# Kernel tuning notes

Hardware: AMD Instinct MI355X
Metric: run time of the kernel (lower is better)

## Reference

```python
import jax, jax.numpy as jnp
import numpy as np

N, E, F_IN, H, O = 50000, 800000, 128, 64, 1


def _gcn_conv(x, row, col, ew, W, b, n_nodes):
    """PyG GCNConv: add self-loops (weight 1), symmetric deg normalization,
    linear transform (no bias inside lin), scatter-add aggregation, then +bias."""
    loop = jnp.arange(n_nodes, dtype=row.dtype)
    r = jnp.concatenate([row, loop])
    c = jnp.concatenate([col, loop])
    w = jnp.concatenate([ew, jnp.ones((n_nodes,), dtype=ew.dtype)])
    deg = jax.ops.segment_sum(w, c, num_segments=n_nodes)            # [N]
    dis = jnp.where(deg > 0, jax.lax.rsqrt(jnp.maximum(deg, 1e-12)), 0.0)
    norm = dis[r] * w * dis[c]                                       # [E+N]
    h = x @ W                                                        # [N, out]
    msg = h[r] * norm[:, None]                                       # gather + scale
    agg = jax.ops.segment_sum(msg, c, num_segments=n_nodes)          # scatter-add
    return agg + b


def setup_inputs() -> dict:
    key = jax.random.key(0)
    ks = jax.random.split(key, 14)
    s = 0.02
    return {
        "x": jax.random.normal(ks[0], (N, F_IN), dtype=jnp.float32),
        "edge_index": jax.random.randint(ks[1], (2, E), 0, N, dtype=jnp.int64),
        "edge_weight": jax.random.uniform(ks[2], (E,), dtype=jnp.float32),
        "W1": jax.random.normal(ks[3], (F_IN, H), dtype=jnp.float32) * s,
        "b1": jnp.zeros((H,), dtype=jnp.float32),
        "W2": jax.random.normal(ks[4], (H, H), dtype=jnp.float32) * s,
        "b2": jnp.zeros((H,), dtype=jnp.float32),
        "W_ih": jax.random.normal(ks[5], (4 * H, H), dtype=jnp.float32) * s,
        "W_hh": jax.random.normal(ks[6], (4 * H, H), dtype=jnp.float32) * s,
        "b_ih": jax.random.normal(ks[7], (4 * H,), dtype=jnp.float32) * s,
        "b_hh": jax.random.normal(ks[8], (4 * H,), dtype=jnp.float32) * s,
        "W_reg": jax.random.normal(ks[9], (H, O), dtype=jnp.float32) * s,
        "b_reg": jnp.zeros((O,), dtype=jnp.float32),
    }


def reference(x, edge_index, edge_weight, W1, b1, W2, b2,
              W_ih, W_hh, b_ih, b_hh, W_reg, b_reg):
    row, col = edge_index[0], edge_index[1]
    n = x.shape[0]
    h = jax.nn.relu(_gcn_conv(x, row, col, edge_weight, W1, b1, n))
    h = jax.nn.relu(_gcn_conv(h, row, col, edge_weight, W2, b2, n))
    # single-step LSTM, zero initial (h0, c0); PyTorch gate order i, f, g, o
    hd = W_ih.shape[1]
    h0 = jnp.zeros((n, hd), dtype=h.dtype)
    gates = h @ W_ih.T + h0 @ W_hh.T + b_ih + b_hh                   # [N, 4H]
    i, f, g, o = jnp.split(gates, 4, axis=-1)
    c = jax.nn.sigmoid(f) * 0.0 + jax.nn.sigmoid(i) * jnp.tanh(g)    # c0 = 0
    hn = jax.nn.sigmoid(o) * jnp.tanh(c)                             # lstm_out[:, -1]
    return hn @ W_reg + b_reg
```

## Files before the change

kernel.cpp:

```cpp
#include <hip/hip_runtime.h>
#include <math.h>


#define QN 6272
#define NOCT 8
#define NPAD (NOCT * QN)
#define NSLICE 128
#define HIST_BLOCKS (NSLICE * NOCT)

__device__ __forceinline__ float sigmoidf_(float x) {
    return 1.0f / (1.0f + expf(-x));
}

__global__ __launch_bounds__(256) void hist_gemm1_k(
        const int* __restrict__ col, unsigned short* __restrict__ part,
        int E, int N,
        const float* __restrict__ x, const float* __restrict__ W1,
        float* __restrict__ C) {
    extern __shared__ char smem[];
    const int t = threadIdx.x;
    if (blockIdx.x < HIST_BLOCKS) {
        int* hc = (int*)smem;
        const int s = blockIdx.x >> 3;
        const int q = blockIdx.x & 7;
        const int lo = q * QN;
        for (int i = t; i < QN; i += 256) hc[i] = 0;
        __syncthreads();
        const int per = (E + NSLICE - 1) / NSLICE;
        const int e0 = s * per, e1 = min(E, e0 + per);
        int e = e0 + t;
        for (; e + 768 < e1; e += 1024) {
            int c0 = col[e], c1 = col[e + 256], c2 = col[e + 512], c3 = col[e + 768];
            unsigned r0 = (unsigned)(c0 - lo), r1 = (unsigned)(c1 - lo);
            unsigned r2 = (unsigned)(c2 - lo), r3 = (unsigned)(c3 - lo);
            if (r0 < (unsigned)QN && (unsigned)c0 < (unsigned)N) atomicAdd(&hc[r0], 1);
            if (r1 < (unsigned)QN && (unsigned)c1 < (unsigned)N) atomicAdd(&hc[r1], 1);
            if (r2 < (unsigned)QN && (unsigned)c2 < (unsigned)N) atomicAdd(&hc[r2], 1);
            if (r3 < (unsigned)QN && (unsigned)c3 < (unsigned)N) atomicAdd(&hc[r3], 1);
        }
        for (; e < e1; e += 256) {
            int c = col[e];
            unsigned rel = (unsigned)(c - lo);
            if (rel < (unsigned)QN && (unsigned)c < (unsigned)N) atomicAdd(&hc[rel], 1);
        }
        __syncthreads();
        unsigned short* dst = part + (size_t)s * NPAD + lo;
        for (int i = t; i < QN; i += 256) dst[i] = (unsigned short)hc[i];
    } else {
        float (*xs)[68] = (float (*)[68])smem;
        float* ws = (float*)(smem + 64 * 68 * sizeof(float));
        const int n0 = (int)(blockIdx.x - HIST_BLOCKS) * 64;
        for (int base = t * 4; base < 128 * 64; base += 1024)
            *(float4*)(ws + base) = *(const float4*)(W1 + base);
        const int cg = t & 15, ng = t >> 4;
        const int colj = cg * 4, nb = ng * 4;
        float acc[4][4];
#pragma unroll
        for (int i = 0; i < 4; ++i)
#pragma unroll
            for (int j = 0; j < 4; ++j) acc[i][j] = 0.0f;
        for (int k0 = 0; k0 < 128; k0 += 64) {
            __syncthreads();
            for (int base = t * 4; base < 64 * 64; base += 1024) {
                int r = base >> 6, k = base & 63;
                int node = n0 + r;
                float4 v = make_float4(0.f, 0.f, 0.f, 0.f);
                if (node < N) v = *(const float4*)(x + (size_t)node * 128 + k0 + k);
                *(float4*)&xs[r][k] = v;
            }
            __syncthreads();
#pragma unroll 4
            for (int kk = 0; kk < 64; kk += 4) {
                float4 a[4];
#pragma unroll
                for (int i = 0; i < 4; ++i) a[i] = *(float4*)&xs[nb + i][kk];
#pragma unroll
                for (int j = 0; j < 4; ++j) {
                    float4 bv = *(float4*)&ws[(size_t)(k0 + kk + j) * 64 + colj];
                    float av[4];
                    switch (j) {
                        case 0: av[0]=a[0].x; av[1]=a[1].x; av[2]=a[2].x; av[3]=a[3].x; break;
                        case 1: av[0]=a[0].y; av[1]=a[1].y; av[2]=a[2].y; av[3]=a[3].y; break;
                        case 2: av[0]=a[0].z; av[1]=a[1].z; av[2]=a[2].z; av[3]=a[3].z; break;
                        default:av[0]=a[0].w; av[1]=a[1].w; av[2]=a[2].w; av[3]=a[3].w; break;
                    }
#pragma unroll
                    for (int i = 0; i < 4; ++i) {
                        acc[i][0] = fmaf(av[i], bv.x, acc[i][0]);
                        acc[i][1] = fmaf(av[i], bv.y, acc[i][1]);
                        acc[i][2] = fmaf(av[i], bv.z, acc[i][2]);
                        acc[i][3] = fmaf(av[i], bv.w, acc[i][3]);
                    }
                }
            }
        }
#pragma unroll
        for (int i = 0; i < 4; ++i) {
            int node = n0 + nb + i;
            if (node < N)
                *(float4*)(C + (size_t)node * 64 + colj) =
                    make_float4(acc[i][0], acc[i][1], acc[i][2], acc[i][3]);
        }
    }
}

__global__ __launch_bounds__(256) void prefixA_k(const unsigned short* __restrict__ part,
                                                 unsigned short* __restrict__ coff,
                                                 int* __restrict__ cnt,
                                                 int* __restrict__ bsum) {
    __shared__ int r[256];
    const int t = threadIdx.x;
    const int i = blockIdx.x * 256 + t;
    int acc = 0;
    for (int s = 0; s < NSLICE; ++s) {
        size_t idx = (size_t)s * NPAD + i;
        coff[idx] = (unsigned short)acc;
        acc += part[idx];
    }
    cnt[i] = acc;
    r[t] = acc;
    __syncthreads();
#pragma unroll
    for (int off = 128; off > 0; off >>= 1) {
        if (t < off) r[t] += r[t + off];
        __syncthreads();
    }
    if (t == 0) bsum[blockIdx.x] = r[0];
}

__global__ __launch_bounds__(256) void scanBC_k(const int* __restrict__ cnt,
                                                const int* __restrict__ bsum,
                                                int* __restrict__ rowptr, int NBLK) {
    __shared__ int s[2][256];
    __shared__ int red[256];
    const int t = threadIdx.x, b = blockIdx.x;
    const int i = b * 256 + t;
    int v = cnt[i];
    int pin = 0;
    s[0][t] = v;
    __syncthreads();
#pragma unroll
    for (int off = 1; off < 256; off <<= 1) {
        int xo = s[pin][t];
        if (t >= off) xo += s[pin][t - off];
        s[pin ^ 1][t] = xo;
        pin ^= 1;
        __syncthreads();
    }
    int excl = s[pin][t] - v;
    red[t] = (t < b && t < NBLK) ? bsum[t] : 0;
    __syncthreads();
#pragma unroll
    for (int off = 128; off > 0; off >>= 1) {
        if (t < off) red[t] += red[t + off];
        __syncthreads();
    }
    rowptr[i] = excl + red[0];
}

__global__ __launch_bounds__(256) void fill_k(const int* __restrict__ row,
                                              const int* __restrict__ col,
                                              const float* __restrict__ ew,
                                              const int* __restrict__ rowptr,
                                              const unsigned short* __restrict__ coff,
                                              int2* __restrict__ pairs, int E, int N) {
    __shared__ int lcur[QN];
    const int t = threadIdx.x;
    const int s = blockIdx.x >> 3;
    const int q = blockIdx.x & 7;
    const int lo = q * QN;
    const unsigned short* cof = coff + (size_t)s * NPAD + lo;
    const int* rp = rowptr + lo;
    for (int i = t; i < QN; i += 256) lcur[i] = rp[i] + (int)cof[i];
    __syncthreads();
    const int per = (E + NSLICE - 1) / NSLICE;
    const int e0 = s * per, e1 = min(E, e0 + per);
    int e = e0 + t;
    for (; e + 768 < e1; e += 1024) {
        int c0 = col[e], c1 = col[e + 256], c2 = col[e + 512], c3 = col[e + 768];
        unsigned r0 = (unsigned)(c0 - lo), r1 = (unsigned)(c1 - lo);
        unsigned r2 = (unsigned)(c2 - lo), r3 = (unsigned)(c3 - lo);
        if (r0 < (unsigned)QN && (unsigned)c0 < (unsigned)N) {
            int r = row[e]; float w = ew[e];
            if ((unsigned)r >= (unsigned)N) { r = 0; w = 0.0f; }
            pairs[atomicAdd(&lcur[r0], 1)] = make_int2(r, __float_as_int(w));
        }
        if (r1 < (unsigned)QN && (unsigned)c1 < (unsigned)N) {
            int r = row[e + 256]; float w = ew[e + 256];
            if ((unsigned)r >= (unsigned)N) { r = 0; w = 0.0f; }
            pairs[atomicAdd(&lcur[r1], 1)] = make_int2(r, __float_as_int(w));
        }
        if (r2 < (unsigned)QN && (unsigned)c2 < (unsigned)N) {
            int r = row[e + 512]; float w = ew[e + 512];
            if ((unsigned)r >= (unsigned)N) { r = 0; w = 0.0f; }
            pairs[atomicAdd(&lcur[r2], 1)] = make_int2(r, __float_as_int(w));
        }
        if (r3 < (unsigned)QN && (unsigned)c3 < (unsigned)N) {
            int r = row[e + 768]; float w = ew[e + 768];
            if ((unsigned)r >= (unsigned)N) { r = 0; w = 0.0f; }
            pairs[atomicAdd(&lcur[r3], 1)] = make_int2(r, __float_as_int(w));
        }
    }
    for (; e < e1; e += 256) {
        int c = col[e];
        unsigned rel = (unsigned)(c - lo);
        if (rel < (unsigned)QN && (unsigned)c < (unsigned)N) {
            int r = row[e]; float w = ew[e];
            if ((unsigned)r >= (unsigned)N) { r = 0; w = 0.0f; }
            pairs[atomicAdd(&lcur[rel], 1)] = make_int2(r, __float_as_int(w));
        }
    }
}

__global__ __launch_bounds__(256) void degsum_k(const int* __restrict__ rowptr,
                                                const int2* __restrict__ pairs,
                                                float* __restrict__ dis, int N) {
    int i = blockIdx.x * 256 + threadIdx.x;
    if (i >= N) return;
    int b = rowptr[i], en = rowptr[i + 1];
    float s = 0.0f;
    for (int e = b; e < en; ++e) s += __int_as_float(pairs[e].y);
    dis[i] = rsqrtf(s + 1.0f);
}

__global__ __launch_bounds__(256) void aggregate_k(const float* __restrict__ h,
                                                   const int* __restrict__ rowptr,
                                                   const int2* __restrict__ pairs,
                                                   const float* __restrict__ dis,
                                                   const float* __restrict__ bias,
                                                   float* __restrict__ out, int N) {
    const int t = threadIdx.x;
    const int lane = t & 63;
    const int n0 = (blockIdx.x * 4 + (t >> 6)) * 4;
    if (n0 >= N) return;

    int rp[5];
#pragma unroll
    for (int k = 0; k < 5; ++k) rp[k] = rowptr[min(n0 + k, N)];
    const int beg = rp[0], end = rp[4];

    float acc[4] = {0.f, 0.f, 0.f, 0.f};
    for (int base = beg; base < end; base += 64) {
        const int m = min(64, end - base);
        int ps = 0; float pv = 0.0f;
        if (lane < m) {
            int2 p = pairs[base + lane];
            ps = p.x;
            pv = __int_as_float(p.y) * dis[p.x];
        }
        const unsigned pu = __float_as_uint(pv);
#pragma unroll
        for (int i = 0; i < 4; ++i) {
            const int s0 = max(rp[i] - base, 0);
            const int s1 = min(rp[i + 1] - base, m);
            int jj = s0;
            for (; jj + 4 <= s1; jj += 4) {
                int a0 = __builtin_amdgcn_readlane(ps, jj);
                int a1 = __builtin_amdgcn_readlane(ps, jj + 1);
                int a2 = __builtin_amdgcn_readlane(ps, jj + 2);
                int a3 = __builtin_amdgcn_readlane(ps, jj + 3);
                float v0 = __uint_as_float(__builtin_amdgcn_readlane(pu, jj));
                float v1 = __uint_as_float(__builtin_amdgcn_readlane(pu, jj + 1));
                float v2 = __uint_as_float(__builtin_amdgcn_readlane(pu, jj + 2));
                float v3 = __uint_as_float(__builtin_amdgcn_readlane(pu, jj + 3));
                float h0 = h[(size_t)a0 * 64 + lane];
                float h1 = h[(size_t)a1 * 64 + lane];
                float h2 = h[(size_t)a2 * 64 + lane];
                float h3 = h[(size_t)a3 * 64 + lane];
                acc[i] = fmaf(h0, v0, acc[i]);
                acc[i] = fmaf(h1, v1, acc[i]);
                acc[i] = fmaf(h2, v2, acc[i]);
                acc[i] = fmaf(h3, v3, acc[i]);
            }
            for (; jj < s1; ++jj) {
                int   a0 = __builtin_amdgcn_readlane(ps, jj);
                float v0 = __uint_as_float(__builtin_amdgcn_readlane(pu, jj));
                acc[i] = fmaf(h[(size_t)a0 * 64 + lane], v0, acc[i]);
            }
        }
    }
#pragma unroll
    for (int i = 0; i < 4; ++i) {
        int node = n0 + i;
        if (node < N) {
            float d = dis[node];
            float a = acc[i];
            a = fmaf(d, h[(size_t)node * 64 + lane], a);
            a = fmaf(d, a, bias[lane]);
            out[(size_t)node * 64 + lane] = fmaxf(a, 0.0f);
        }
    }
}

template <int K>
__global__ __launch_bounds__(256) void gemm64_k(const float* __restrict__ A,
                                                const float* __restrict__ W,
                                                float* __restrict__ C, int M) {
    __shared__ float xs[64][68];
    __shared__ float ws[K][64];
    const int t  = threadIdx.x;
    const int n0 = blockIdx.x * 64;

    for (int base = t * 4; base < K * 64; base += 1024)
        *(float4*)((float*)ws + base) = *(const float4*)(W + base);

    const int cg = t & 15, ng = t >> 4;
    const int col = cg * 4, nb = ng * 4;
    float acc[4][4];
#pragma unroll
    for (int i = 0; i < 4; ++i)
#pragma unroll
        for (int j = 0; j < 4; ++j) acc[i][j] = 0.0f;

    for (int k0 = 0; k0 < K; k0 += 64) {
        __syncthreads();
        for (int base = t * 4; base < 64 * 64; base += 1024) {
            int r = base >> 6, k = base & 63;
            int node = n0 + r;
            float4 v = make_float4(0.f, 0.f, 0.f, 0.f);
            if (node < M) v = *(const float4*)(A + (size_t)node * K + k0 + k);
            *(float4*)&xs[r][k] = v;
        }
        __syncthreads();
#pragma unroll 4
        for (int kk = 0; kk < 64; kk += 4) {
            float4 a[4];
#pragma unroll
            for (int i = 0; i < 4; ++i) a[i] = *(float4*)&xs[nb + i][kk];
#pragma unroll
            for (int j = 0; j < 4; ++j) {
                float4 bv = *(float4*)&ws[k0 + kk + j][col];
                float av[4];
                switch (j) {
                    case 0: av[0]=a[0].x; av[1]=a[1].x; av[2]=a[2].x; av[3]=a[3].x; break;
                    case 1: av[0]=a[0].y; av[1]=a[1].y; av[2]=a[2].y; av[3]=a[3].y; break;
                    case 2: av[0]=a[0].z; av[1]=a[1].z; av[2]=a[2].z; av[3]=a[3].z; break;
                    default:av[0]=a[0].w; av[1]=a[1].w; av[2]=a[2].w; av[3]=a[3].w; break;
                }
#pragma unroll
                for (int i = 0; i < 4; ++i) {
                    acc[i][0] = fmaf(av[i], bv.x, acc[i][0]);
                    acc[i][1] = fmaf(av[i], bv.y, acc[i][1]);
                    acc[i][2] = fmaf(av[i], bv.z, acc[i][2]);
                    acc[i][3] = fmaf(av[i], bv.w, acc[i][3]);
                }
            }
        }
    }
#pragma unroll
    for (int i = 0; i < 4; ++i) {
        int node = n0 + nb + i;
        if (node < M)
            *(float4*)(C + (size_t)node * 64 + col) =
                make_float4(acc[i][0], acc[i][1], acc[i][2], acc[i][3]);
    }
}

__global__ __launch_bounds__(256) void lstm_head_k(const float* __restrict__ h,
                                                   const float* __restrict__ Wih,
                                                   const float* __restrict__ bih,
                                                   const float* __restrict__ bhh,
                                                   const float* __restrict__ Wreg,
                                                   const float* __restrict__ breg,
                                                   float* __restrict__ out, int N) {
    __shared__ float wt[64 * 192];
    __shared__ float hsT[64 * 64];
    const int t = threadIdx.x;
    const int n0 = blockIdx.x * 64;

    {
        const int j = t & 63, kq = (t >> 6) * 4;
#pragma unroll
        for (int gid = 0; gid < 3; ++gid) {
            const int gBase = (gid == 0) ? 0 : (gid == 1 ? 128 : 192);
            const int gOff = gid * 64;
#pragma unroll
            for (int it = 0; it < 4; ++it) {
                int k0 = it * 16 + kq;
                float4 w = *(const float4*)(Wih + (size_t)(gBase + j) * 64 + k0);
                wt[(k0 + 0) * 192 + gOff + j] = w.x;
                wt[(k0 + 1) * 192 + gOff + j] = w.y;
                wt[(k0 + 2) * 192 + gOff + j] = w.z;
                wt[(k0 + 3) * 192 + gOff + j] = w.w;
            }
        }
    }
    {
        const int r = t & 63, kq = (t >> 6) * 4;
        const int node = n0 + r;
#pragma unroll
        for (int it = 0; it < 4; ++it) {
            int k0 = it * 16 + kq;
            float4 v = make_float4(0.f, 0.f, 0.f, 0.f);
            if (node < N) v = *(const float4*)(h + (size_t)node * 64 + k0);
            hsT[(k0 + 0) * 64 + r] = v.x;
            hsT[(k0 + 1) * 64 + r] = v.y;
            hsT[(k0 + 2) * 64 + r] = v.z;
            hsT[(k0 + 3) * 64 + r] = v.w;
        }
    }

    const int cg = t & 15, ng = t >> 4;
    const int col = cg * 4, nb = ng * 4;
    float4 bi4 = *(const float4*)(bih + col);
    float4 bg4 = *(const float4*)(bih + 128 + col);
    float4 bo4 = *(const float4*)(bih + 192 + col);
    {
        float4 h0 = *(const float4*)(bhh + col);
        float4 h1 = *(const float4*)(bhh + 128 + col);
        float4 h2 = *(const float4*)(bhh + 192 + col);
        bi4.x += h0.x; bi4.y += h0.y; bi4.z += h0.z; bi4.w += h0.w;
        bg4.x += h1.x; bg4.y += h1.y; bg4.z += h1.z; bg4.w += h1.w;
        bo4.x += h2.x; bo4.y += h2.y; bo4.z += h2.z; bo4.w += h2.w;
    }
    float4 wr4 = *(const float4*)(Wreg + col);
    const float br = breg[0];

    __syncthreads();

    float ai[4][4], ag[4][4], ao[4][4];
#pragma unroll
    for (int i = 0; i < 4; ++i)
#pragma unroll
        for (int j = 0; j < 4; ++j) { ai[i][j] = 0.f; ag[i][j] = 0.f; ao[i][j] = 0.f; }

#pragma unroll 4
    for (int k = 0; k < 64; ++k) {
        float4 a  = *(float4*)&hsT[k * 64 + nb];
        float4 wi = *(float4*)&wt[k * 192 + col];
        float4 wg = *(float4*)&wt[k * 192 + 64 + col];
        float4 wo = *(float4*)&wt[k * 192 + 128 + col];
        const float av[4] = {a.x, a.y, a.z, a.w};
#pragma unroll
        for (int i = 0; i < 4; ++i) {
            ai[i][0] = fmaf(av[i], wi.x, ai[i][0]);
            ai[i][1] = fmaf(av[i], wi.y, ai[i][1]);
            ai[i][2] = fmaf(av[i], wi.z, ai[i][2]);
            ai[i][3] = fmaf(av[i], wi.w, ai[i][3]);
            ag[i][0] = fmaf(av[i], wg.x, ag[i][0]);
            ag[i][1] = fmaf(av[i], wg.y, ag[i][1]);
            ag[i][2] = fmaf(av[i], wg.z, ag[i][2]);
            ag[i][3] = fmaf(av[i], wg.w, ag[i][3]);
            ao[i][0] = fmaf(av[i], wo.x, ao[i][0]);
            ao[i][1] = fmaf(av[i], wo.y, ao[i][1]);
            ao[i][2] = fmaf(av[i], wo.z, ao[i][2]);
            ao[i][3] = fmaf(av[i], wo.w, ao[i][3]);
        }
    }

    const float bia[4] = {bi4.x, bi4.y, bi4.z, bi4.w};
    const float bga[4] = {bg4.x, bg4.y, bg4.z, bg4.w};
    const float boa[4] = {bo4.x, bo4.y, bo4.z, bo4.w};
    const float wra[4] = {wr4.x, wr4.y, wr4.z, wr4.w};
    float res[4];
#pragma unroll
    for (int i = 0; i < 4; ++i) {
        float s = 0.f;
#pragma unroll
        for (int j = 0; j < 4; ++j) {
            float gi = ai[i][j] + bia[j];
            float gg = ag[i][j] + bga[j];
            float go = ao[i][j] + boa[j];
            float cc = sigmoidf_(gi) * tanhf(gg);
            float hn = sigmoidf_(go) * tanhf(cc);
            s = fmaf(hn, wra[j], s);
        }
        res[i] = s;
    }
#pragma unroll
    for (int off = 8; off > 0; off >>= 1) {
#pragma unroll
        for (int i = 0; i < 4; ++i) res[i] += __shfl_down(res[i], off);
    }
    if (cg == 0) {
#pragma unroll
        for (int i = 0; i < 4; ++i) {
            int node = n0 + nb + i;
            if (node < N) out[node] = res[i] + br;
        }
    }
}

extern "C" void kernel_launch(void* const* d_in, const int* in_sizes, int n_in,
                              void* d_out, int out_size, void* d_ws, size_t ws_size,
                              hipStream_t stream) {
    const float* x    = (const float*)d_in[0];
    const int*   ei   = (const int*)d_in[1];
    const float* ew   = (const float*)d_in[2];
    const float* W1   = (const float*)d_in[3];
    const float* b1   = (const float*)d_in[4];
    const float* W2   = (const float*)d_in[5];
    const float* b2   = (const float*)d_in[6];
    const float* Wih  = (const float*)d_in[7];
    const float* bih  = (const float*)d_in[9];
    const float* bhh  = (const float*)d_in[10];
    const float* Wreg = (const float*)d_in[11];
    const float* breg = (const float*)d_in[12];
    float* out = (float*)d_out;

    const int N = out_size;
    const int E = in_sizes[1] / 2;
    const int* row = ei;
    const int* col = ei + E;

    const int NB   = (N + 255) / 256;
    const int NBLK = NPAD / 256;

    char* wsb = (char*)d_ws;
    size_t off = 0;
    unsigned short* part = (unsigned short*)(wsb + off); off += (size_t)NSLICE * NPAD * 2;
    unsigned short* coff = (unsigned short*)(wsb + off); off += (size_t)NSLICE * NPAD * 2;
    float* bufA   = (float*)(wsb + off); off += (size_t)N * 64 * 4;
    float* bufB   = (float*)(wsb + off); off += (size_t)N * 64 * 4;
    float* bufC   = (float*)(wsb + off); off += (size_t)N * 64 * 4;
    int2*  pairs  = (int2*) (wsb + off); off += (size_t)E * 8;
    float* dis    = (float*)(wsb + off); off += (size_t)NPAD * 4;
    int*   cnt    = (int*)  (wsb + off); off += (size_t)NPAD * 4;
    int*   rowptr = (int*)  (wsb + off); off += ((size_t)NPAD + 64) * 4;
    int*   bsum   = (int*)  (wsb + off); off += 1024;

    const int gb = (N + 63) / 64;
    const int ab = (N + 15) / 16;
    const size_t DSM = 64 * 68 * sizeof(float) + 128 * 64 * sizeof(float);

    hist_gemm1_k<<<HIST_BLOCKS + gb, 256, DSM, stream>>>(col, part, E, N, x, W1, bufA);
    prefixA_k<<<NBLK, 256, 0, stream>>>(part, coff, cnt, bsum);
    scanBC_k<<<NBLK, 256, 0, stream>>>(cnt, bsum, rowptr, NBLK);
    fill_k<<<HIST_BLOCKS, 256, 0, stream>>>(row, col, ew, rowptr, coff, pairs, E, N);
    degsum_k<<<NB, 256, 0, stream>>>(rowptr, pairs, dis, N);
    aggregate_k<<<ab, 256, 0, stream>>>(bufA, rowptr, pairs, dis, b1, bufB, N);
    gemm64_k<64><<<gb, 256, 0, stream>>>(bufB, W2, bufC, N);
    aggregate_k<<<ab, 256, 0, stream>>>(bufC, rowptr, pairs, dis, b2, bufA, N);
    lstm_head_k<<<gb, 256, 0, stream>>>(bufA, Wih, bih, bhh, Wreg, breg, out, N);
}
```

Measured before the change: 272.2 us.

## Pack local destination index into pairs and balance aggregation edges across block waves

The CSR build now stores each edge's destination index within its 16-node group in the upper bits of the source-row field. The aggregation kernel splits a block's 16-node edge range evenly across its four waves instead of giving each wave four fixed nodes. Partial sums go into a shared-memory accumulator through LDS float atomics, then an epilogue applies self-loop, normalization, bias and ReLU. This evens out per-wave work under skewed degrees, at the cost of one LDS atomic per edge per lane and extra masking.

Result: slower. 758.6 us (+178.7%).

```diff
diff --git a/kernel.cpp b/kernel.cpp
--- a/kernel.cpp
+++ b/kernel.cpp
@@ -183,22 +183,26 @@
         if (r0 < (unsigned)QN && (unsigned)c0 < (unsigned)N) {
             int r = row[e]; float w = ew[e];
             if ((unsigned)r >= (unsigned)N) { r = 0; w = 0.0f; }
-            pairs[atomicAdd(&lcur[r0], 1)] = make_int2(r, __float_as_int(w));
+            pairs[atomicAdd(&lcur[r0], 1)] =
+                make_int2(r | ((c0 & 15) << 20), __float_as_int(w));
         }
         if (r1 < (unsigned)QN && (unsigned)c1 < (unsigned)N) {
             int r = row[e + 256]; float w = ew[e + 256];
             if ((unsigned)r >= (unsigned)N) { r = 0; w = 0.0f; }
-            pairs[atomicAdd(&lcur[r1], 1)] = make_int2(r, __float_as_int(w));
+            pairs[atomicAdd(&lcur[r1], 1)] =
+                make_int2(r | ((c1 & 15) << 20), __float_as_int(w));
         }
         if (r2 < (unsigned)QN && (unsigned)c2 < (unsigned)N) {
             int r = row[e + 512]; float w = ew[e + 512];
             if ((unsigned)r >= (unsigned)N) { r = 0; w = 0.0f; }
-            pairs[atomicAdd(&lcur[r2], 1)] = make_int2(r, __float_as_int(w));
+            pairs[atomicAdd(&lcur[r2], 1)] =
+                make_int2(r | ((c2 & 15) << 20), __float_as_int(w));
         }
         if (r3 < (unsigned)QN && (unsigned)c3 < (unsigned)N) {
             int r = row[e + 768]; float w = ew[e + 768];
             if ((unsigned)r >= (unsigned)N) { r = 0; w = 0.0f; }
-            pairs[atomicAdd(&lcur[r3], 1)] = make_int2(r, __float_as_int(w));
+            pairs[atomicAdd(&lcur[r3], 1)] =
+                make_int2(r | ((c3 & 15) << 20), __float_as_int(w));
         }
     }
     for (; e < e1; e += 256) {
@@ -207,7 +211,8 @@
         if (rel < (unsigned)QN && (unsigned)c < (unsigned)N) {
             int r = row[e]; float w = ew[e];
             if ((unsigned)r >= (unsigned)N) { r = 0; w = 0.0f; }
-            pairs[atomicAdd(&lcur[rel], 1)] = make_int2(r, __float_as_int(w));
+            pairs[atomicAdd(&lcur[rel], 1)] =
+                make_int2(r | ((c & 15) << 20), __float_as_int(w));
         }
     }
 }
@@ -229,65 +234,63 @@
                                                    const float* __restrict__ dis,
                                                    const float* __restrict__ bias,
                                                    float* __restrict__ out, int N) {
+    __shared__ float acc[16 * 64];
     const int t = threadIdx.x;
-    const int lane = t & 63;
-    const int n0 = (blockIdx.x * 4 + (t >> 6)) * 4;
+    const int lane = t & 63, w = t >> 6;
+    const int n0 = blockIdx.x * 16;
     if (n0 >= N) return;
 
-    int rp[5];
-#pragma unroll
-    for (int k = 0; k < 5; ++k) rp[k] = rowptr[min(n0 + k, N)];
-    const int beg = rp[0], end = rp[4];
-
-    float acc[4] = {0.f, 0.f, 0.f, 0.f};
-    for (int base = beg; base < end; base += 64) {
-        const int m = min(64, end - base);
-        int ps = 0; float pv = 0.0f;
+    for (int i = t; i < 16 * 64; i += 256) acc[i] = 0.0f;
+    const int eb = rowptr[n0];
+    const int ee = rowptr[min(n0 + 16, N)];
+    __syncthreads();
+
+    for (int base = eb + w * 64; base < ee; base += 256) {
+        const int m = min(64, ee - base);
+        int pp = 0; float pv = 0.0f;
         if (lane < m) {
             int2 p = pairs[base + lane];
-            ps = p.x;
-            pv = __int_as_float(p.y) * dis[p.x];
+            pp = p.x;
+            pv = __int_as_float(p.y) * dis[p.x & 0xFFFFF];
         }
         const unsigned pu = __float_as_uint(pv);
-#pragma unroll
-        for (int i = 0; i < 4; ++i) {
-            const int s0 = max(rp[i] - base, 0);
-            const int s1 = min(rp[i + 1] - base, m);
-            int jj = s0;
-            for (; jj + 4 <= s1; jj += 4) {
-                int a0 = __builtin_amdgcn_readlane(ps, jj);
-                int a1 = __builtin_amdgcn_readlane(ps, jj + 1);
-                int a2 = __builtin_amdgcn_readlane(ps, jj + 2);
-                int a3 = __builtin_amdgcn_readlane(ps, jj + 3);
-                float v0 = __uint_as_float(__builtin_amdgcn_readlane(pu, jj));
-                float v1 = __uint_as_float(__builtin_amdgcn_readlane(pu, jj + 1));
-                float v2 = __uint_as_float(__builtin_amdgcn_readlane(pu, jj + 2));
-                float v3 = __uint_as_float(__builtin_amdgcn_readlane(pu, jj + 3));
-                float h0 = h[(size_t)a0 * 64 + lane];
-                float h1 = h[(size_t)a1 * 64 + lane];
-                float h2 = h[(size_t)a2 * 64 + lane];
-                float h3 = h[(size_t)a3 * 64 + lane];
-                acc[i] = fmaf(h0, v0, acc[i]);
-                acc[i] = fmaf(h1, v1, acc[i]);
-                acc[i] = fmaf(h2, v2, acc[i]);
-                acc[i] = fmaf(h3, v3, acc[i]);
-            }
-            for (; jj < s1; ++jj) {
-                int   a0 = __builtin_amdgcn_readlane(ps, jj);
-                float v0 = __uint_as_float(__builtin_amdgcn_readlane(pu, jj));
-                acc[i] = fmaf(h[(size_t)a0 * 64 + lane], v0, acc[i]);
-            }
-        }
-    }
-#pragma unroll
-    for (int i = 0; i < 4; ++i) {
-        int node = n0 + i;
+        int j = 0;
+        for (; j + 4 <= m; j += 4) {
+            int q0 = __builtin_amdgcn_readlane(pp, j);
+            int q1 = __builtin_amdgcn_readlane(pp, j + 1);
+            int q2 = __builtin_amdgcn_readlane(pp, j + 2);
+            int q3 = __builtin_amdgcn_readlane(pp, j + 3);
+            float v0 = __uint_as_float(__builtin_amdgcn_readlane(pu, j));
+            float v1 = __uint_as_float(__builtin_amdgcn_readlane(pu, j + 1));
+            float v2 = __uint_as_float(__builtin_amdgcn_readlane(pu, j + 2));
+            float v3 = __uint_as_float(__builtin_amdgcn_readlane(pu, j + 3));
+            float h0 = h[(size_t)(q0 & 0xFFFFF) * 64 + lane];
+            float h1 = h[(size_t)(q1 & 0xFFFFF) * 64 + lane];
+            float h2 = h[(size_t)(q2 & 0xFFFFF) * 64 + lane];
+            float h3 = h[(size_t)(q3 & 0xFFFFF) * 64 + lane];
+            atomicAdd(&acc[((q0 >> 20) << 6) + lane], h0 * v0);
+            atomicAdd(&acc[((q1 >> 20) << 6) + lane], h1 * v1);
+            atomicAdd(&acc[((q2 >> 20) << 6) + lane], h2 * v2);
+            atomicAdd(&acc[((q3 >> 20) << 6) + lane], h3 * v3);
+        }
+        for (; j < m; ++j) {
+            int q0 = __builtin_amdgcn_readlane(pp, j);
+            float v0 = __uint_as_float(__builtin_amdgcn_readlane(pu, j));
+            atomicAdd(&acc[((q0 >> 20) << 6) + lane],
+                      h[(size_t)(q0 & 0xFFFFF) * 64 + lane] * v0);
+        }
+    }
+    __syncthreads();
+
+    for (int idx = t; idx < 16 * 64; idx += 256) {
+        int node = n0 + (idx >> 6);
+        int f = idx & 63;
         if (node < N) {
             float d = dis[node];
-            float a = acc[i];
-            a = fmaf(d, h[(size_t)node * 64 + lane], a);
-            a = fmaf(d, a, bias[lane]);
-            out[(size_t)node * 64 + lane] = fmaxf(a, 0.0f);
+            float a = acc[idx];
+            a = fmaf(d, h[(size_t)node * 64 + f], a);
+            a = fmaf(d, a, bias[f]);
+            out[(size_t)node * 64 + f] = fmaxf(a, 0.0f);
         }
     }
 }
```
